# Optimization experiments

Measured on AMD Instinct MI355X. Metric: run time of the kernel, lower is better.

Reference implementation:

```python
import jax, jax.numpy as jnp
import numpy as np

B, N, F_IN, D = 32768, 4, 512, 64  # N fixed to 4 by the max_pool(4,1)+reshape


def setup_inputs() -> dict:
    key = jax.random.key(0)
    k1, k2, k3, k4 = jax.random.split(key, 4)
    scale = 1.0 / np.sqrt(F_IN)
    return {
        "drug": jax.random.normal(k1, (B, N, F_IN), dtype=jnp.float32),
        "Wk": jax.random.normal(k2, (F_IN, D), dtype=jnp.float32) * scale,
        "Wq": jax.random.normal(k3, (F_IN, D), dtype=jnp.float32) * scale,
        "Wv": jax.random.normal(k4, (F_IN, D), dtype=jnp.float32) * scale,
    }


def reference(drug, Wk, Wq, Wv):
    # projections: torch nn.Linear(bias=False) -> x @ W  (W stored as [in, out] here)
    k = jnp.einsum("bnf,fd->bnd", drug, Wk)
    q = jnp.einsum("bnf,fd->bnd", drug, Wq)
    v = jnp.einsum("bnf,fd->bnd", drug, Wv)
    # score = bmm(K, Q^T); NOTE: no 1/sqrt(d) scaling, matching the source
    score = jnp.einsum("bnd,bmd->bnm", k, q)  # [B, N, N]
    attn = jax.nn.softmax(score, axis=2)
    out = jnp.einsum("bnm,bmd->bnd", attn, v)  # [B, N, D]
    # max_pool2d kernel (4,1), stride (4,1) over N=4 -> max over axis 1, then reshape [B, D]
    return jnp.max(out, axis=1)
```

## Files before the change

### kernel.cpp

```cpp
#include <hip/hip_runtime.h>
#include <hip/hip_fp16.h>

#define BTOT   32768
#define FIN    512
#define NCOLS  192
#define KSTEPS 16
#define NTILES 12
#define WH_ELEMS (KSTEPS * NTILES * 64 * 8)
#define CHUNK_HALVES (NTILES * 64 * 8)
#define CHUNK_BYTES  (CHUNK_HALVES * 2)
#define PHASES 8

using half8   = __attribute__((ext_vector_type(8))) _Float16;
using floatx4 = __attribute__((ext_vector_type(4))) float;

#define GLOAD_LDS16(gp, lp)                                                  \
    __builtin_amdgcn_global_load_lds(                                        \
        (const __attribute__((address_space(1))) void*)(gp),                 \
        (__attribute__((address_space(3))) void*)(lp), 16, 0, 0)

__global__ void convert_w_kernel(const float* __restrict__ Wk,
                                 const float* __restrict__ Wq,
                                 const float* __restrict__ Wv,
                                 _Float16* __restrict__ Wh) {
    int idx = blockIdx.x * blockDim.x + threadIdx.x;
    if (idx >= WH_ELEMS) return;
    int j    = idx & 7;
    int lane = (idx >> 3) & 63;
    int t    = (idx >> 9) % NTILES;
    int kk   = idx / CHUNK_HALVES;
    int k = kk * 32 + (lane >> 4) * 8 + j;
    int n = t * 16 + (lane & 15);
    const float* src = (n < 64) ? Wk : (n < 128) ? Wq : Wv;
    Wh[idx] = (_Float16)src[k * 64 + (n & 63)];
}

__global__ __launch_bounds__(256, 3) void attn_fused_kernel(
        const float* __restrict__ drug,
        const _Float16* __restrict__ Wh,
        float* __restrict__ out)
{
    __shared__ __align__(16) char lds[2 * CHUNK_BYTES];

    const int tid  = threadIdx.x;
    const int wave = tid >> 6;
    const int lane = tid & 63;
    const int quad = lane >> 4;
    const int l15  = lane & 15;

    const int row = blockIdx.x * 64 + wave * 16 + l15;
    const float* arow = drug + (size_t)row * FIN + quad * 8;
    const char* gW = (const char*)Wh;

    half8 afrag[KSTEPS];
#pragma unroll
    for (int kk = 0; kk < KSTEPS; ++kk) {
        const float4* ap = (const float4*)(arow + kk * 32);
        float4 a0 = ap[0];
        float4 a1 = ap[1];
        afrag[kk][0] = (_Float16)a0.x; afrag[kk][1] = (_Float16)a0.y;
        afrag[kk][2] = (_Float16)a0.z; afrag[kk][3] = (_Float16)a0.w;
        afrag[kk][4] = (_Float16)a1.x; afrag[kk][5] = (_Float16)a1.y;
        afrag[kk][6] = (_Float16)a1.z; afrag[kk][7] = (_Float16)a1.w;
    }

    floatx4 acc[NTILES];
#pragma unroll
    for (int t = 0; t < NTILES; ++t) acc[t] = (floatx4){0.f, 0.f, 0.f, 0.f};

#pragma unroll
    for (int ph = 0; ph < PHASES; ++ph) {
        __syncthreads();

        const size_t goff = (size_t)ph * 2 * CHUNK_BYTES;
#pragma unroll
        for (int i = 0; i < 6; ++i) {
            const int off = i * 4096 + wave * 1024;
            GLOAD_LDS16(gW + goff + off + lane * 16, lds + off);
        }

        __syncthreads();

#pragma unroll
        for (int s = 0; s < 2; ++s) {
            const _Float16* lh = (const _Float16*)(lds + s * CHUNK_BYTES);
#pragma unroll
            for (int t = 0; t < NTILES; ++t) {
                half8 bfrag = *((const half8*)(lh + (t * 64 + lane) * 8));
                acc[t] = __builtin_amdgcn_mfma_f32_16x16x32_f16(afrag[2 * ph + s], bfrag, acc[t], 0, 0, 0);
            }
        }
    }

    float p[4][4];
#pragma unroll
    for (int n = 0; n < 4; ++n)
#pragma unroll
        for (int m = 0; m < 4; ++m) {
            float s = 0.f;
#pragma unroll
            for (int t = 0; t < 4; ++t) s += acc[t][n] * acc[4 + t][m];
            p[n][m] = s;
        }

#pragma unroll
    for (int mask = 1; mask < 16; mask <<= 1) {
#pragma unroll
        for (int n = 0; n < 4; ++n)
#pragma unroll
            for (int m = 0; m < 4; ++m)
                p[n][m] += __shfl_xor(p[n][m], mask, 64);
    }

    float res[4] = {-INFINITY, -INFINITY, -INFINITY, -INFINITY};
#pragma unroll
    for (int n = 0; n < 4; ++n) {
        float mx = fmaxf(fmaxf(p[n][0], p[n][1]), fmaxf(p[n][2], p[n][3]));
        float e0 = __expf(p[n][0] - mx);
        float e1 = __expf(p[n][1] - mx);
        float e2 = __expf(p[n][2] - mx);
        float e3 = __expf(p[n][3] - mx);
        float inv = 1.f / (e0 + e1 + e2 + e3);
#pragma unroll
        for (int t = 0; t < 4; ++t) {
            float o = (e0 * acc[8 + t][0] + e1 * acc[8 + t][1] +
                       e2 * acc[8 + t][2] + e3 * acc[8 + t][3]) * inv;
            res[t] = fmaxf(res[t], o);
        }
    }

    const int b = blockIdx.x * 16 + wave * 4 + quad;
#pragma unroll
    for (int t = 0; t < 4; ++t)
        out[b * 64 + t * 16 + l15] = res[t];
}

extern "C" void kernel_launch(void* const* d_in, const int* in_sizes, int n_in,
                              void* d_out, int out_size, void* d_ws, size_t ws_size,
                              hipStream_t stream) {
    const float* drug = (const float*)d_in[0];
    const float* Wk   = (const float*)d_in[1];
    const float* Wq   = (const float*)d_in[2];
    const float* Wv   = (const float*)d_in[3];
    float* out = (float*)d_out;
    _Float16* Wh = (_Float16*)d_ws;

    convert_w_kernel<<<(WH_ELEMS + 255) / 256, 256, 0, stream>>>(Wk, Wq, Wv, Wh);
    attn_fused_kernel<<<BTOT / 16, 256, 0, stream>>>(drug, Wh, out);
}
```

Measured before the change: 391.1 us.

## Stage most fp16 weights once per persistent block, stream remaining k-steps from global

Replaces the per-block phased double-buffer weight staging with persistent 512-thread blocks. Each block loads 12 of the 16 k-steps of the converted fp16 weights into LDS once (about 144 KB) and loops over two row groups per wave. The last 4 k-steps are read directly from global/L2. The A rows are kept as fp32 in registers and converted per k-step. This removes repeated weight reloads and the per-phase barriers, in exchange for large LDS use, higher register pressure, and a fixed grid of 512 blocks.

```diff
diff --git a/kernel.cpp b/kernel.cpp
--- a/kernel.cpp
+++ b/kernel.cpp
@@ -3,13 +3,13 @@
 
 #define BTOT   32768
 #define FIN    512
-#define NCOLS  192
 #define KSTEPS 16
 #define NTILES 12
+#define LDS_KSTEPS 12
 #define WH_ELEMS (KSTEPS * NTILES * 64 * 8)
 #define CHUNK_HALVES (NTILES * 64 * 8)
 #define CHUNK_BYTES  (CHUNK_HALVES * 2)
-#define PHASES 8
+#define LDS_BYTES    (LDS_KSTEPS * CHUNK_BYTES)
 
 using half8   = __attribute__((ext_vector_type(8))) _Float16;
 using floatx4 = __attribute__((ext_vector_type(4))) float;
@@ -35,12 +35,12 @@
     Wh[idx] = (_Float16)src[k * 64 + (n & 63)];
 }
 
-__global__ __launch_bounds__(256, 3) void attn_fused_kernel(
+__global__ __launch_bounds__(512, 2) void attn_fused_kernel(
         const float* __restrict__ drug,
         const _Float16* __restrict__ Wh,
         float* __restrict__ out)
 {
-    __shared__ __align__(16) char lds[2 * CHUNK_BYTES];
+    __shared__ __align__(16) char lds[LDS_BYTES];
 
     const int tid  = threadIdx.x;
     const int wave = tid >> 6;
@@ -48,91 +48,106 @@
     const int quad = lane >> 4;
     const int l15  = lane & 15;
 
-    const int row = blockIdx.x * 64 + wave * 16 + l15;
-    const float* arow = drug + (size_t)row * FIN + quad * 8;
-    const char* gW = (const char*)Wh;
+    {
+        const char* gW = (const char*)Wh;
+#pragma unroll
+        for (int i = 0; i < 18; ++i) {
+            const int off = i * 8192 + wave * 1024;
+            GLOAD_LDS16(gW + off + lane * 16, lds + off);
+        }
+    }
+    __syncthreads();
 
-    half8 afrag[KSTEPS];
+#pragma unroll 1
+    for (int it = 0; it < 2; ++it) {
+        const int gw  = blockIdx.x * 8 + wave + it * 4096;
+        const int row = gw * 16 + l15;
+        const float* arow = drug + (size_t)row * FIN + quad * 8;
+
+        float4 areg[KSTEPS][2];
 #pragma unroll
-    for (int kk = 0; kk < KSTEPS; ++kk) {
-        const float4* ap = (const float4*)(arow + kk * 32);
-        float4 a0 = ap[0];
-        float4 a1 = ap[1];
-        afrag[kk][0] = (_Float16)a0.x; afrag[kk][1] = (_Float16)a0.y;
-        afrag[kk][2] = (_Float16)a0.z; afrag[kk][3] = (_Float16)a0.w;
-        afrag[kk][4] = (_Float16)a1.x; afrag[kk][5] = (_Float16)a1.y;
-        afrag[kk][6] = (_Float16)a1.z; afrag[kk][7] = (_Float16)a1.w;
-    }
+        for (int kk = 0; kk < KSTEPS; ++kk) {
+            const float4* ap = (const float4*)(arow + kk * 32);
+            areg[kk][0] = ap[0];
+            areg[kk][1] = ap[1];
+        }
 
-    floatx4 acc[NTILES];
+        floatx4 acc[NTILES];
 #pragma unroll
-    for (int t = 0; t < NTILES; ++t) acc[t] = (floatx4){0.f, 0.f, 0.f, 0.f};
+        for (int t = 0; t < NTILES; ++t) acc[t] = (floatx4){0.f, 0.f, 0.f, 0.f};
 
 #pragma unroll
-    for (int ph = 0; ph < PHASES; ++ph) {
-        __syncthreads();
-
-        const size_t goff = (size_t)ph * 2 * CHUNK_BYTES;
-#pragma unroll
-        for (int i = 0; i < 6; ++i) {
-            const int off = i * 4096 + wave * 1024;
-            GLOAD_LDS16(gW + goff + off + lane * 16, lds + off);
-        }
-
-        __syncthreads();
-
-#pragma unroll
-        for (int s = 0; s < 2; ++s) {
-            const _Float16* lh = (const _Float16*)(lds + s * CHUNK_BYTES);
+        for (int kk = 0; kk < LDS_KSTEPS; ++kk) {
+            half8 afrag;
+            afrag[0] = (_Float16)areg[kk][0].x; afrag[1] = (_Float16)areg[kk][0].y;
+            afrag[2] = (_Float16)areg[kk][0].z; afrag[3] = (_Float16)areg[kk][0].w;
+            afrag[4] = (_Float16)areg[kk][1].x; afrag[5] = (_Float16)areg[kk][1].y;
+            afrag[6] = (_Float16)areg[kk][1].z; afrag[7] = (_Float16)areg[kk][1].w;
+            const _Float16* lh = (const _Float16*)(lds + kk * CHUNK_BYTES);
 #pragma unroll
             for (int t = 0; t < NTILES; ++t) {
                 half8 bfrag = *((const half8*)(lh + (t * 64 + lane) * 8));
-                acc[t] = __builtin_amdgcn_mfma_f32_16x16x32_f16(afrag[2 * ph + s], bfrag, acc[t], 0, 0, 0);
+                acc[t] = __builtin_amdgcn_mfma_f32_16x16x32_f16(afrag, bfrag, acc[t], 0, 0, 0);
             }
-        }
-    }
-
-    float p[4][4];
-#pragma unroll
-    for (int n = 0; n < 4; ++n)
-#pragma unroll
-        for (int m = 0; m < 4; ++m) {
-            float s = 0.f;
-#pragma unroll
-            for (int t = 0; t < 4; ++t) s += acc[t][n] * acc[4 + t][m];
-            p[n][m] = s;
         }
 
 #pragma unroll
-    for (int mask = 1; mask < 16; mask <<= 1) {
+        for (int kk = LDS_KSTEPS; kk < KSTEPS; ++kk) {
+            half8 afrag;
+            afrag[0] = (_Float16)areg[kk][0].x; afrag[1] = (_Float16)areg[kk][0].y;
+            afrag[2] = (_Float16)areg[kk][0].z; afrag[3] = (_Float16)areg[kk][0].w;
+            afrag[4] = (_Float16)areg[kk][1].x; afrag[5] = (_Float16)areg[kk][1].y;
+            afrag[6] = (_Float16)areg[kk][1].z; afrag[7] = (_Float16)areg[kk][1].w;
+            const half8* gb = (const half8*)(Wh + kk * CHUNK_HALVES + lane * 8);
+#pragma unroll
+            for (int t = 0; t < NTILES; ++t) {
+                half8 bfrag = gb[t * 64];
+                acc[t] = __builtin_amdgcn_mfma_f32_16x16x32_f16(afrag, bfrag, acc[t], 0, 0, 0);
+            }
+        }
+
+        float p[4][4];
 #pragma unroll
         for (int n = 0; n < 4; ++n)
 #pragma unroll
-            for (int m = 0; m < 4; ++m)
-                p[n][m] += __shfl_xor(p[n][m], mask, 64);
+            for (int m = 0; m < 4; ++m) {
+                float s = 0.f;
+#pragma unroll
+                for (int t = 0; t < 4; ++t) s += acc[t][n] * acc[4 + t][m];
+                p[n][m] = s;
+            }
+
+#pragma unroll
+        for (int mask = 1; mask < 16; mask <<= 1) {
+#pragma unroll
+            for (int n = 0; n < 4; ++n)
+#pragma unroll
+                for (int m = 0; m < 4; ++m)
+                    p[n][m] += __shfl_xor(p[n][m], mask, 64);
+        }
+
+        float res[4] = {-INFINITY, -INFINITY, -INFINITY, -INFINITY};
+#pragma unroll
+        for (int n = 0; n < 4; ++n) {
+            float mx = fmaxf(fmaxf(p[n][0], p[n][1]), fmaxf(p[n][2], p[n][3]));
+            float e0 = __expf(p[n][0] - mx);
+            float e1 = __expf(p[n][1] - mx);
+            float e2 = __expf(p[n][2] - mx);
+            float e3 = __expf(p[n][3] - mx);
+            float inv = 1.f / (e0 + e1 + e2 + e3);
+#pragma unroll
+            for (int t = 0; t < 4; ++t) {
+                float o = (e0 * acc[8 + t][0] + e1 * acc[8 + t][1] +
+                           e2 * acc[8 + t][2] + e3 * acc[8 + t][3]) * inv;
+                res[t] = fmaxf(res[t], o);
+            }
+        }
+
+        const int b = gw * 4 + quad;
+#pragma unroll
+        for (int t = 0; t < 4; ++t)
+            out[b * 64 + t * 16 + l15] = res[t];
     }
-
-    float res[4] = {-INFINITY, -INFINITY, -INFINITY, -INFINITY};
-#pragma unroll
-    for (int n = 0; n < 4; ++n) {
-        float mx = fmaxf(fmaxf(p[n][0], p[n][1]), fmaxf(p[n][2], p[n][3]));
-        float e0 = __expf(p[n][0] - mx);
-        float e1 = __expf(p[n][1] - mx);
-        float e2 = __expf(p[n][2] - mx);
-        float e3 = __expf(p[n][3] - mx);
-        float inv = 1.f / (e0 + e1 + e2 + e3);
-#pragma unroll
-        for (int t = 0; t < 4; ++t) {
-            float o = (e0 * acc[8 + t][0] + e1 * acc[8 + t][1] +
-                       e2 * acc[8 + t][2] + e3 * acc[8 + t][3]) * inv;
-            res[t] = fmaxf(res[t], o);
-        }
-    }
-
-    const int b = blockIdx.x * 16 + wave * 4 + quad;
-#pragma unroll
-    for (int t = 0; t < 4; ++t)
-        out[b * 64 + t * 16 + l15] = res[t];
 }
 
 extern "C" void kernel_launch(void* const* d_in, const int* in_sizes, int n_in,
@@ -146,5 +161,5 @@
     _Float16* Wh = (_Float16*)d_ws;
 
     convert_w_kernel<<<(WH_ELEMS + 255) / 256, 256, 0, stream>>>(Wk, Wq, Wv, Wh);
-    attn_fused_kernel<<<BTOT / 16, 256, 0, stream>>>(drug, Wh, out);
+    attn_fused_kernel<<<512, 512, 0, stream>>>(drug, Wh, out);
 }
```

Result: slower. 823.7 us (+110.6%).
